# Performance work log

Hardware: AMD Instinct MI355X
Metric: run time of the kernel (lower is better)

## Reference

```python
import jax, jax.numpy as jnp
import numpy as np

B = 4
IN_DIM = 512
HID = 1024
MLP_LAYERS = 2
SEQ = 4096          # output_dim / sequence_length
RH = 64             # ripl_hidden_dim
RL = 2              # ripl_num_layers
MULT = 1            # ripl_coordinate_multipler

MID_DIM = 2 * RH * RH + (RH + 1) * RH      # per middle ripple layer param count
OUT_DIM = 2 * RH * 1 + (RH + 1) * 1        # output ripple layer param count
MLP_OUT = RL * MID_DIM + OUT_DIM


def gelu(x):
    return jax.nn.gelu(x, approximate=False)


def layer_norm(x, g, b, eps=1e-5):
    mu = jnp.mean(x, axis=-1, keepdims=True)
    var = jnp.var(x, axis=-1, keepdims=True)
    return (x - mu) * jax.lax.rsqrt(var + eps) * g + b


def batch_ripple(x, w, b):
    # x: (B,S,I), w: (B,O,I,2), b: (B,O,I+1)
    # out[b,s,o] = b[b,o,0] + sum_i b[b,o,i+1] * sin(w[b,o,i,0]*x[b,s,i] + w[b,o,i,1])
    arg = w[:, None, :, :, 0] * x[:, :, None, :] + w[:, None, :, :, 1]  # (B,S,O,I)
    return b[:, None, :, 0] + jnp.sum(jnp.sin(arg) * b[:, None, :, 1:], axis=-1)


def setup_inputs() -> dict:
    key = jax.random.key(0)
    ks = jax.random.split(key, 20)
    s = 0.02
    inp = {
        "x": jax.random.normal(ks[0], (B, IN_DIM), jnp.float32),
        "mlp_w0": jax.random.normal(ks[1], (IN_DIM, HID), jnp.float32) * s,
        "mlp_b0": jnp.zeros((HID,), jnp.float32),
        "mlp_w1": jax.random.normal(ks[2], (HID, HID), jnp.float32) * s,
        "mlp_b1": jnp.zeros((HID,), jnp.float32),
        "ln_g1": jnp.ones((HID,), jnp.float32),
        "ln_b1": jnp.zeros((HID,), jnp.float32),
        "mlp_w2": jax.random.normal(ks[3], (HID, HID), jnp.float32) * s,
        "mlp_b2": jnp.zeros((HID,), jnp.float32),
        "ln_g2": jnp.ones((HID,), jnp.float32),
        "ln_b2": jnp.zeros((HID,), jnp.float32),
        "mlp_w3": jax.random.normal(ks[4], (HID, MLP_OUT), jnp.float32) * s,
        "mlp_b3": jnp.zeros((MLP_OUT,), jnp.float32),
        "lc_w": jax.random.normal(ks[5], (1, RH), jnp.float32) * 0.1,
        "lc_b": jax.random.normal(ks[6], (RH,), jnp.float32) * 0.1,
        "byp_w": jax.random.normal(ks[7], (1, 1, 2), jnp.float32),
        "byp_b": jax.random.normal(ks[8], (1, 2), jnp.float32),
    }
    return inp


def reference(x, mlp_w0, mlp_b0, mlp_w1, mlp_b1, ln_g1, ln_b1,
              mlp_w2, mlp_b2, ln_g2, ln_b2, mlp_w3, mlp_b3,
              lc_w, lc_b, byp_w, byp_b):
    # hypernetwork MLP: Linear+GELU, [Linear+LN+GELU]*2, Linear
    h = gelu(x @ mlp_w0 + mlp_b0)
    h = gelu(layer_norm(h @ mlp_w1 + mlp_b1, ln_g1, ln_b1))
    h = gelu(layer_norm(h @ mlp_w2 + mlp_b2, ln_g2, ln_b2))
    mlp_out = h @ mlp_w3 + mlp_b3                      # (B, MLP_OUT)

    # split into RL middle ripple layers then the output layer
    middles = [mlp_out[:, i * MID_DIM:(i + 1) * MID_DIM] for i in range(RL)]
    out_w = mlp_out[:, RL * MID_DIM:RL * MID_DIM + OUT_DIM]

    # line coordinates -> fc layer
    lc = (jnp.arange(SEQ, dtype=jnp.float32) * MULT)[None, :, None]  # (1,S,1)
    lc = jnp.broadcast_to(lc, (x.shape[0], SEQ, 1))
    lc_x = lc @ lc_w + lc_b                                          # (B,S,RH)
    lc_bypass = lc_x

    for mw in middles:
        w = mw[:, :2 * RH * RH].reshape(-1, RH, RH, 2)
        b = mw[:, 2 * RH * RH:].reshape(-1, RH, RH + 1)
        lc_x = gelu(batch_ripple(lc_x, w, b))

    wo = out_w[:, :2 * RH].reshape(-1, 1, RH, 2)
    bo = out_w[:, 2 * RH:].reshape(-1, 1, RH + 1)
    lc_x = batch_ripple(lc_x, wo, bo)                                # (B,S,1)

    # learned RippleLinear(1,1) bypass, broadcast over features then reduced
    byp = byp_b[0, 0] + jnp.sum(
        jnp.sin(byp_w[0, 0, 0] * lc_bypass + byp_w[0, 0, 1]) * byp_b[0, 1],
        axis=-1, keepdims=True)
    lc_x = lc_x + byp
    return jnp.transpose(lc_x, (0, 2, 1))                            # (B,1,S)
```

## Files before the change

kernel.cpp:

```cpp
#include <hip/hip_runtime.h>
#include <hip/hip_bf16.h>
#include <math.h>

#define B_      4
#define IN_DIM  512
#define HID     1024
#define SEQ     4096
#define RH      64
#define RL      2
#define MID_DIM 12352
#define OUT_DIM 193
#define MLP_OUT 24897
#define INV2PI  0.15915494309189535f

#define MLPT_STRIDE 25088

#define OFF_P0    0
#define OFF_P1    32768
#define OFF_H1    98304
#define OFF_P2    102400
#define OFF_H2    167936
#define OFF_P3    172032
#define OFF_MLPT  968736

__device__ __forceinline__ float gelu_exact(float v) {
    return 0.5f * v * (1.0f + erff(v * 0.70710678118654752f));
}

__device__ __forceinline__ float hw_sin_rev(float r) {
    r = r - __builtin_rintf(r);
    return __builtin_amdgcn_sinf(r);
}

__global__ void k_gemm0(const float* __restrict__ x, const float* __restrict__ w0,
                        float* __restrict__ p0) {
    const int cch = blockIdx.x;
    const int kc  = blockIdx.y;
    const int tid = threadIdx.x;
    __shared__ float xs[256];
    {
        const int b = tid >> 6, k = tid & 63;
        xs[tid] = x[b * IN_DIM + kc * 64 + k];
    }
    __syncthreads();
    const int b = tid >> 6, cl = tid & 63;
    const int c = cch * 64 + cl;
    const float* wp = w0 + (size_t)(kc * 64) * HID + c;
    const float* xp = xs + b * 64;
    float acc = 0.f;
    #pragma unroll 8
    for (int k = 0; k < 64; ++k)
        acc = fmaf(xp[k], wp[(size_t)k * HID], acc);
    p0[(kc * 4 + b) * HID + c] = acc;
}

__global__ void k_gemm1(const float* __restrict__ p0, const float* __restrict__ b0,
                        const float* __restrict__ w1, float* __restrict__ p1) {
    const int cch = blockIdx.x;
    const int kc  = blockIdx.y;
    const int tid = threadIdx.x;
    __shared__ float hs[256];
    {
        const int b = tid >> 6, k = tid & 63;
        const int kg = kc * 64 + k;
        float v = b0[kg];
        #pragma unroll
        for (int j = 0; j < 8; ++j) v += p0[(j * 4 + b) * HID + kg];
        hs[tid] = gelu_exact(v);
    }
    __syncthreads();
    const int b = tid >> 6, cl = tid & 63;
    const int c = cch * 64 + cl;
    const float* wp = w1 + (size_t)(kc * 64) * HID + c;
    const float* hp = hs + b * 64;
    float acc = 0.f;
    #pragma unroll 8
    for (int k = 0; k < 64; ++k)
        acc = fmaf(hp[k], wp[(size_t)k * HID], acc);
    p1[(kc * 4 + b) * HID + c] = acc;
}

__global__ void k_gemm2(const float* __restrict__ h, const float* __restrict__ w,
                        float* __restrict__ pout) {
    const int cch = blockIdx.x;
    const int kc  = blockIdx.y;
    const int tid = threadIdx.x;
    __shared__ float hs[256];
    {
        const int b = tid >> 6, k = tid & 63;
        hs[tid] = h[b * HID + kc * 64 + k];
    }
    __syncthreads();
    const int b = tid >> 6, cl = tid & 63;
    const int c = cch * 64 + cl;
    const float* wp = w + (size_t)(kc * 64) * HID + c;
    const float* hp = hs + b * 64;
    float acc = 0.f;
    #pragma unroll 8
    for (int k = 0; k < 64; ++k)
        acc = fmaf(hp[k], wp[(size_t)k * HID], acc);
    pout[(kc * 4 + b) * HID + c] = acc;
}

__global__ void k_lng(const float* __restrict__ part, const float* __restrict__ bias,
                      const float* __restrict__ g, const float* __restrict__ bl,
                      float* __restrict__ h) {
    const int b = blockIdx.x, tid = threadIdx.x;
    float v = bias[tid];
    #pragma unroll
    for (int j = 0; j < 16; ++j) v += part[(j * 4 + b) * HID + tid];
    float s1 = v, s2 = v * v;
    #pragma unroll
    for (int m = 1; m < 64; m <<= 1) {
        s1 += __shfl_xor(s1, m, 64);
        s2 += __shfl_xor(s2, m, 64);
    }
    __shared__ float r1[16], r2[16], s_mu, s_rs;
    const int lane = tid & 63, wid = tid >> 6;
    if (lane == 0) { r1[wid] = s1; r2[wid] = s2; }
    __syncthreads();
    if (tid == 0) {
        float a = 0.f, c = 0.f;
        #pragma unroll
        for (int j = 0; j < 16; ++j) { a += r1[j]; c += r2[j]; }
        const float mu = a * (1.0f / HID);
        s_mu = mu;
        s_rs = rsqrtf(c * (1.0f / HID) - mu * mu + 1e-5f);
    }
    __syncthreads();
    h[b * HID + tid] = gelu_exact((v - s_mu) * s_rs * g[tid] + bl[tid]);
}

__global__ void k_gemm3(const float* __restrict__ h2, const float* __restrict__ w3,
                        float* __restrict__ p3) {
    const int cch = blockIdx.x;
    const int kc  = blockIdx.y;
    const int tid = threadIdx.x;
    __shared__ float hs[512];
    for (int e = tid; e < 512; e += 256) {
        const int b = e >> 7, k = e & 127;
        hs[e] = h2[b * HID + kc * 128 + k];
    }
    __syncthreads();
    const int c = cch * 256 + tid;
    if (c >= MLP_OUT) return;
    const float* wp = w3 + (size_t)(kc * 128) * MLP_OUT + c;
    float a0 = 0.f, a1 = 0.f, a2 = 0.f, a3 = 0.f;
    #pragma unroll 16
    for (int k = 0; k < 128; ++k) {
        const float w = wp[(size_t)k * MLP_OUT];
        a0 = fmaf(hs[k],       w, a0);
        a1 = fmaf(hs[128 + k], w, a1);
        a2 = fmaf(hs[256 + k], w, a2);
        a3 = fmaf(hs[384 + k], w, a3);
    }
    p3[(size_t)(kc * 4 + 0) * MLP_OUT + c] = a0;
    p3[(size_t)(kc * 4 + 1) * MLP_OUT + c] = a1;
    p3[(size_t)(kc * 4 + 2) * MLP_OUT + c] = a2;
    p3[(size_t)(kc * 4 + 3) * MLP_OUT + c] = a3;
}

__global__ void k_comb3T(const float* __restrict__ p3, const float* __restrict__ b3,
                         float* __restrict__ mlpT) {
    const int d = blockIdx.x * 256 + threadIdx.x;
    const int b = blockIdx.y;
    int src = -1;
    float scale = 1.f;
    if (d < 24832) {
        const int l = d / 12416, r = d % 12416;
        const int base = l * MID_DIM;
        if (r < 8192) {
            const int half = r >> 12;
            const int rr = r & 4095;
            const int i = rr >> 6, o = rr & 63;
            src = base + o * 128 + i * 2 + half;
            scale = INV2PI;
        } else if (r < 12288) {
            const int rr = r - 8192;
            const int i = rr >> 6, o = rr & 63;
            src = base + 8192 + o * 65 + 1 + i;
        } else if (r < 12352) {
            const int o = r - 12288;
            src = base + 8192 + o * 65;
        }
    } else {
        const int rr = d - 24832;
        const int base = RL * MID_DIM;
        if (rr < 64)        { src = base + rr * 2;            scale = INV2PI; }
        else if (rr < 128)  { src = base + (rr - 64) * 2 + 1; scale = INV2PI; }
        else if (rr < 192)  { src = base + 128 + 1 + (rr - 128); }
        else if (rr == 192) { src = base + 128; }
    }
    float v = 0.f;
    if (src >= 0) {
        v = b3[src];
        #pragma unroll
        for (int j = 0; j < 8; ++j) v += p3[(size_t)(j * 4 + b) * MLP_OUT + src];
        v *= scale;
    }
    mlpT[(size_t)b * MLPT_STRIDE + d] = v;
}

__global__ void __launch_bounds__(256, 2) k_ripple(
        const float* __restrict__ mlpT, const float* __restrict__ lcw,
        const float* __restrict__ lcb, const float* __restrict__ bypw,
        const float* __restrict__ bypb, float* __restrict__ out) {
    const int tid = threadIdx.x;
    const int b = blockIdx.y;
    const int t0 = blockIdx.x * 32;
    const int lane = tid & 63, wid = tid >> 6, tb = wid * 8;

    __shared__ __align__(16) float s_w[12416];
    __shared__ __align__(16) float s_x[64 * 36];
    __shared__ __align__(16) float s_wo[256];
    __shared__ float s_red[32];

    const float* mb = mlpT + (size_t)b * MLPT_STRIDE;

    {
        const float4* src = reinterpret_cast<const float4*>(mb);
        float4* dst = reinterpret_cast<float4*>(s_w);
        for (int e = tid; e < 3104; e += 256) dst[e] = src[e];
        if (tid < 64) {
            reinterpret_cast<float4*>(s_wo)[tid] =
                reinterpret_cast<const float4*>(mb + 24832)[tid];
        }
    }
    const float lw = lcw[lane], lb = lcb[lane];
    for (int e = tid; e < 2048; e += 256) {
        const int i = e >> 5, tt = e & 31;
        s_x[i * 36 + tt] = fmaf((float)(t0 + tt), lcw[i], lcb[i]);
    }
    __syncthreads();

    float acc[8];
    for (int layer = 0; layer < 2; ++layer) {
        const float bc = s_w[12288 + lane];
        #pragma unroll
        for (int j = 0; j < 8; ++j) acc[j] = bc;
        for (int i = 0; i < 64; ++i) {
            const float ws = s_w[i * 64 + lane];
            const float wo = s_w[4096 + i * 64 + lane];
            const float bs = s_w[8192 + i * 64 + lane];
            const float4 xa = *reinterpret_cast<const float4*>(&s_x[i * 36 + tb]);
            const float4 xb = *reinterpret_cast<const float4*>(&s_x[i * 36 + tb + 4]);
            const float xv[8] = {xa.x, xa.y, xa.z, xa.w, xb.x, xb.y, xb.z, xb.w};
            #pragma unroll
            for (int j = 0; j < 8; ++j) {
                const float r = fmaf(ws, xv[j], wo);
                acc[j] = fmaf(hw_sin_rev(r), bs, acc[j]);
            }
        }
        __syncthreads();
        if (layer == 0) {
            #pragma unroll
            for (int j = 0; j < 8; ++j)
                s_x[lane * 36 + tb + j] = gelu_exact(acc[j]);
            const float4* src = reinterpret_cast<const float4*>(mb + 12416);
            float4* dst = reinterpret_cast<float4*>(s_w);
            for (int e = tid; e < 3104; e += 256) dst[e] = src[e];
            __syncthreads();
        }
    }

    {
        const float wsO = s_wo[lane], woO = s_wo[64 + lane], bsO = s_wo[128 + lane];
        const float bcO = s_wo[192];
        const float bw0 = bypw[0] * INV2PI, bw1 = bypw[1] * INV2PI;
        const float bb0 = bypb[0], bb1 = bypb[1];
        #pragma unroll
        for (int j = 0; j < 8; ++j) {
            const int t = t0 + tb + j;
            const float v = gelu_exact(acc[j]);
            float s = hw_sin_rev(fmaf(wsO, v, woO)) * bsO;
            const float xb = fmaf((float)t, lw, lb);
            s = fmaf(hw_sin_rev(fmaf(bw0, xb, bw1)), bb1, s);
            #pragma unroll
            for (int m = 1; m < 64; m <<= 1) s += __shfl_xor(s, m, 64);
            if (lane == 0) s_red[tb + j] = s + bcO + bb0;
        }
    }
    __syncthreads();
    if (tid < 32) out[(size_t)b * SEQ + t0 + tid] = s_red[tid];
}

extern "C" void kernel_launch(void* const* d_in, const int* in_sizes, int n_in,
                              void* d_out, int out_size, void* d_ws, size_t ws_size,
                              hipStream_t stream) {
    const float* x     = (const float*)d_in[0];
    const float* w0    = (const float*)d_in[1];
    const float* b0    = (const float*)d_in[2];
    const float* w1    = (const float*)d_in[3];
    const float* b1    = (const float*)d_in[4];
    const float* g1    = (const float*)d_in[5];
    const float* bln1  = (const float*)d_in[6];
    const float* w2    = (const float*)d_in[7];
    const float* b2    = (const float*)d_in[8];
    const float* g2    = (const float*)d_in[9];
    const float* bln2  = (const float*)d_in[10];
    const float* w3    = (const float*)d_in[11];
    const float* b3    = (const float*)d_in[12];
    const float* lcw   = (const float*)d_in[13];
    const float* lcb   = (const float*)d_in[14];
    const float* bypw  = (const float*)d_in[15];
    const float* bypb  = (const float*)d_in[16];
    float* out = (float*)d_out;
    float* ws  = (float*)d_ws;

    float* p0   = ws + OFF_P0;
    float* p1   = ws + OFF_P1;
    float* h1   = ws + OFF_H1;
    float* p2   = ws + OFF_P2;
    float* h2   = ws + OFF_H2;
    float* p3   = ws + OFF_P3;
    float* mlpT = ws + OFF_MLPT;

    k_gemm0 <<<dim3(16, 8),  256, 0, stream>>>(x,  w0, p0);
    k_gemm1 <<<dim3(16, 16), 256, 0, stream>>>(p0, b0, w1, p1);
    k_lng   <<<B_, 1024,     0, stream>>>(p1, b1, g1, bln1, h1);
    k_gemm2 <<<dim3(16, 16), 256, 0, stream>>>(h1, w2, p2);
    k_lng   <<<B_, 1024,     0, stream>>>(p2, b2, g2, bln2, h2);
    k_gemm3 <<<dim3(98, 8),  256, 0, stream>>>(h2, w3, p3);
    k_comb3T<<<dim3(98, B_), 256, 0, stream>>>(p3, b3, mlpT);
    k_ripple<<<dim3(SEQ / 32, B_), 256, 0, stream>>>(mlpT, lcw, lcb, bypw, bypb, out);
}
```

Measured before the change: 262.5 us.

## Fuse MLP and ripple stages into one cooperative persistent kernel with grid syncs

Replaces the eight separate launches with one cooperative kernel of 512 blocks that runs each stage in turn, separated by grid.sync(). Gemm3 is restructured so each block covers all of K for 64 columns, reducing partials in shared memory and writing the transposed, pre-scaled ripple parameters directly, which removes the separate combine kernel and the p3 round trip. The goal is to cut launch overhead and inter-kernel gaps. In exchange there are several grid-wide barriers, and occupancy is limited by about 60KB of shared memory per block. If the cooperative launch fails, it falls back to the multi-kernel path.

```diff
diff --git a/kernel.cpp b/kernel.cpp
--- a/kernel.cpp
+++ b/kernel.cpp
@@ -1,6 +1,8 @@
 #include <hip/hip_runtime.h>
-#include <hip/hip_bf16.h>
+#include <hip/hip_cooperative_groups.h>
 #include <math.h>
+
+namespace cg = cooperative_groups;
 
 #define B_      4
 #define IN_DIM  512
@@ -12,7 +14,6 @@
 #define OUT_DIM 193
 #define MLP_OUT 24897
 #define INV2PI  0.15915494309189535f
-
 #define MLPT_STRIDE 25088
 
 #define OFF_P0    0
@@ -20,8 +21,8 @@
 #define OFF_H1    98304
 #define OFF_P2    102400
 #define OFF_H2    167936
-#define OFF_P3    172032
-#define OFF_MLPT  968736
+#define OFF_MLPT  172032
+#define OFF_P3F   272384
 
 __device__ __forceinline__ float gelu_exact(float v) {
     return 0.5f * v * (1.0f + erff(v * 0.70710678118654752f));
@@ -32,16 +33,271 @@
     return __builtin_amdgcn_sinf(r);
 }
 
+__device__ __forceinline__ void lng_phase(const float* __restrict__ part,
+                                          const float* __restrict__ bias,
+                                          const float* __restrict__ g,
+                                          const float* __restrict__ bl,
+                                          float* __restrict__ h,
+                                          int b, int tid, float* smem) {
+    float v[4];
+    float s1 = 0.f, s2 = 0.f;
+    #pragma unroll
+    for (int q = 0; q < 4; ++q) {
+        const int col = q * 256 + tid;
+        float t = bias[col];
+        #pragma unroll
+        for (int j = 0; j < 16; ++j) t += part[(j * 4 + b) * HID + col];
+        v[q] = t; s1 += t; s2 += t * t;
+    }
+    #pragma unroll
+    for (int m = 1; m < 64; m <<= 1) {
+        s1 += __shfl_xor(s1, m, 64);
+        s2 += __shfl_xor(s2, m, 64);
+    }
+    const int lane = tid & 63, wid = tid >> 6;
+    if (lane == 0) { smem[wid] = s1; smem[4 + wid] = s2; }
+    __syncthreads();
+    if (tid == 0) {
+        float a = 0.f, c = 0.f;
+        #pragma unroll
+        for (int j = 0; j < 4; ++j) { a += smem[j]; c += smem[4 + j]; }
+        const float mu = a * (1.0f / HID);
+        smem[8] = mu;
+        smem[9] = rsqrtf(c * (1.0f / HID) - mu * mu + 1e-5f);
+    }
+    __syncthreads();
+    const float mu = smem[8], rs = smem[9];
+    #pragma unroll
+    for (int q = 0; q < 4; ++q) {
+        const int col = q * 256 + tid;
+        h[b * HID + col] = gelu_exact((v[q] - mu) * rs * g[col] + bl[col]);
+    }
+}
+
+__global__ void __launch_bounds__(256, 2) k_fused(
+        const float* __restrict__ x,   const float* __restrict__ w0,
+        const float* __restrict__ b0,  const float* __restrict__ w1,
+        const float* __restrict__ b1,  const float* __restrict__ g1,
+        const float* __restrict__ bl1, const float* __restrict__ w2,
+        const float* __restrict__ b2,  const float* __restrict__ g2,
+        const float* __restrict__ bl2, const float* __restrict__ w3,
+        const float* __restrict__ b3,  const float* __restrict__ lcw,
+        const float* __restrict__ lcb, const float* __restrict__ bypw,
+        const float* __restrict__ bypb, float* __restrict__ out,
+        float* __restrict__ ws) {
+    cg::grid_group grid = cg::this_grid();
+    const int bid = blockIdx.x;
+    const int tid = threadIdx.x;
+    __shared__ __align__(16) float smem[15008];
+
+    float* p0   = ws + OFF_P0;
+    float* p1   = ws + OFF_P1;
+    float* h1   = ws + OFF_H1;
+    float* p2   = ws + OFF_P2;
+    float* h2   = ws + OFF_H2;
+    float* mlpT = ws + OFF_MLPT;
+
+    if (bid < 128) {
+        const int kc = bid >> 4, cch = bid & 15;
+        float* xs = smem;
+        { const int b = tid >> 6, k = tid & 63; xs[tid] = x[b * IN_DIM + kc * 64 + k]; }
+        __syncthreads();
+        const int b = tid >> 6, cl = tid & 63;
+        const int c = cch * 64 + cl;
+        const float* wp = w0 + (size_t)(kc * 64) * HID + c;
+        const float* xp = xs + b * 64;
+        float acc = 0.f;
+        #pragma unroll 8
+        for (int k = 0; k < 64; ++k) acc = fmaf(xp[k], wp[(size_t)k * HID], acc);
+        p0[(kc * 4 + b) * HID + c] = acc;
+    }
+    grid.sync();
+
+    if (bid < 256) {
+        const int kc = bid >> 4, cch = bid & 15;
+        float* hs = smem;
+        {
+            const int b = tid >> 6, k = tid & 63;
+            const int kg = kc * 64 + k;
+            float v = b0[kg];
+            #pragma unroll
+            for (int j = 0; j < 8; ++j) v += p0[(j * 4 + b) * HID + kg];
+            hs[tid] = gelu_exact(v);
+        }
+        __syncthreads();
+        const int b = tid >> 6, cl = tid & 63;
+        const int c = cch * 64 + cl;
+        const float* wp = w1 + (size_t)(kc * 64) * HID + c;
+        const float* hp = hs + b * 64;
+        float acc = 0.f;
+        #pragma unroll 8
+        for (int k = 0; k < 64; ++k) acc = fmaf(hp[k], wp[(size_t)k * HID], acc);
+        p1[(kc * 4 + b) * HID + c] = acc;
+    }
+    grid.sync();
+
+    if (bid < 4) lng_phase(p1, b1, g1, bl1, h1, bid, tid, smem);
+    grid.sync();
+
+    if (bid < 256) {
+        const int kc = bid >> 4, cch = bid & 15;
+        float* hs = smem;
+        {
+            const int b = tid >> 6, k = tid & 63;
+            hs[tid] = h1[b * HID + kc * 64 + k];
+        }
+        __syncthreads();
+        const int b = tid >> 6, cl = tid & 63;
+        const int c = cch * 64 + cl;
+        const float* wp = w2 + (size_t)(kc * 64) * HID + c;
+        const float* hp = hs + b * 64;
+        float acc = 0.f;
+        #pragma unroll 8
+        for (int k = 0; k < 64; ++k) acc = fmaf(hp[k], wp[(size_t)k * HID], acc);
+        p2[(kc * 4 + b) * HID + c] = acc;
+    }
+    grid.sync();
+
+    if (bid < 4) lng_phase(p2, b2, g2, bl2, h2, bid, tid, smem);
+    grid.sync();
+
+    if (bid < 390) {
+        float* sh  = smem;
+        float* red = smem + 4096;
+        for (int e = tid; e < 4096; e += 256) sh[e] = h2[e];
+        __syncthreads();
+        const int cl = tid & 63, kg = tid >> 6;
+        const int c = bid * 64 + cl;
+        float a0 = 0.f, a1 = 0.f, a2 = 0.f, a3 = 0.f;
+        if (c < MLP_OUT) {
+            const float* wp = w3 + (size_t)(kg * 256) * MLP_OUT + c;
+            const float* h0 = sh + kg * 256;
+            #pragma unroll 16
+            for (int k = 0; k < 256; ++k) {
+                const float w = wp[(size_t)k * MLP_OUT];
+                a0 = fmaf(h0[k],        w, a0);
+                a1 = fmaf(h0[1024 + k], w, a1);
+                a2 = fmaf(h0[2048 + k], w, a2);
+                a3 = fmaf(h0[3072 + k], w, a3);
+            }
+        }
+        red[(kg * 4 + 0) * 64 + cl] = a0;
+        red[(kg * 4 + 1) * 64 + cl] = a1;
+        red[(kg * 4 + 2) * 64 + cl] = a2;
+        red[(kg * 4 + 3) * 64 + cl] = a3;
+        __syncthreads();
+        if (c < MLP_OUT) {
+            float v = b3[c];
+            #pragma unroll
+            for (int j = 0; j < 4; ++j) v += red[(j * 4 + kg) * 64 + cl];
+            int d; float scale = 1.f;
+            if (c < RL * MID_DIM) {
+                const int l = c / MID_DIM, r = c % MID_DIM;
+                if (r < 8192) {
+                    const int o = r >> 7, rem = r & 127;
+                    d = l * 12416 + (rem & 1) * 4096 + (rem >> 1) * 64 + o;
+                    scale = INV2PI;
+                } else {
+                    const int u = r - 8192;
+                    const int o = u / 65, idx = u % 65;
+                    d = l * 12416 + (idx == 0 ? 12288 + o : 8192 + (idx - 1) * 64 + o);
+                }
+            } else {
+                const int u = c - RL * MID_DIM;
+                if (u < 128)      { d = 24832 + (u & 1) * 64 + (u >> 1); scale = INV2PI; }
+                else if (u == 128){ d = 24832 + 192; }
+                else              { d = 24832 + 128 + (u - 129); }
+            }
+            mlpT[(size_t)kg * MLPT_STRIDE + d] = v * scale;
+        }
+    }
+    grid.sync();
+
+    {
+        const int b  = bid & 3;
+        const int t0 = (bid >> 2) * 32;
+        const int lane = tid & 63, wid = tid >> 6, tb = wid * 8;
+
+        float* s_w   = smem;
+        float* s_x   = smem + 12416;
+        float* s_wo  = smem + 14720;
+        float* s_red = smem + 14976;
+
+        const float* mb = mlpT + (size_t)b * MLPT_STRIDE;
+
+        {
+            const float4* src = reinterpret_cast<const float4*>(mb);
+            float4* dst = reinterpret_cast<float4*>(s_w);
+            for (int e = tid; e < 3104; e += 256) dst[e] = src[e];
+            if (tid < 64) {
+                reinterpret_cast<float4*>(s_wo)[tid] =
+                    reinterpret_cast<const float4*>(mb + 24832)[tid];
+            }
+        }
+        const float lw = lcw[lane], lb = lcb[lane];
+        for (int e = tid; e < 2048; e += 256) {
+            const int i = e >> 5, tt = e & 31;
+            s_x[i * 36 + tt] = fmaf((float)(t0 + tt), lcw[i], lcb[i]);
+        }
+        __syncthreads();
+
+        float acc[8];
+        for (int layer = 0; layer < 2; ++layer) {
+            const float bc = s_w[12288 + lane];
+            #pragma unroll
+            for (int j = 0; j < 8; ++j) acc[j] = bc;
+            for (int i = 0; i < 64; ++i) {
+                const float ws_ = s_w[i * 64 + lane];
+                const float wo_ = s_w[4096 + i * 64 + lane];
+                const float bs_ = s_w[8192 + i * 64 + lane];
+                const float4 xa = *reinterpret_cast<const float4*>(&s_x[i * 36 + tb]);
+                const float4 xb = *reinterpret_cast<const float4*>(&s_x[i * 36 + tb + 4]);
+                const float xv[8] = {xa.x, xa.y, xa.z, xa.w, xb.x, xb.y, xb.z, xb.w};
+                #pragma unroll
+                for (int j = 0; j < 8; ++j) {
+                    const float r = fmaf(ws_, xv[j], wo_);
+                    acc[j] = fmaf(hw_sin_rev(r), bs_, acc[j]);
+                }
+            }
+            __syncthreads();
+            if (layer == 0) {
+                #pragma unroll
+                for (int j = 0; j < 8; ++j)
+                    s_x[lane * 36 + tb + j] = gelu_exact(acc[j]);
+                const float4* src = reinterpret_cast<const float4*>(mb + 12416);
+                float4* dst = reinterpret_cast<float4*>(s_w);
+                for (int e = tid; e < 3104; e += 256) dst[e] = src[e];
+                __syncthreads();
+            }
+        }
+
+        {
+            const float wsO = s_wo[lane], woO = s_wo[64 + lane], bsO = s_wo[128 + lane];
+            const float bcO = s_wo[192];
+            const float bw0 = bypw[0] * INV2PI, bw1 = bypw[1] * INV2PI;
+            const float bb0 = bypb[0], bb1 = bypb[1];
+            #pragma unroll
+            for (int j = 0; j < 8; ++j) {
+                const int t = t0 + tb + j;
+                const float v = gelu_exact(acc[j]);
+                float s = hw_sin_rev(fmaf(wsO, v, woO)) * bsO;
+                const float xbv = fmaf((float)t, lw, lb);
+                s = fmaf(hw_sin_rev(fmaf(bw0, xbv, bw1)), bb1, s);
+                #pragma unroll
+                for (int m = 1; m < 64; m <<= 1) s += __shfl_xor(s, m, 64);
+                if (lane == 0) s_red[tb + j] = s + bcO + bb0;
+            }
+        }
+        __syncthreads();
+        if (tid < 32) out[(size_t)b * SEQ + t0 + tid] = s_red[tid];
+    }
+}
+
 __global__ void k_gemm0(const float* __restrict__ x, const float* __restrict__ w0,
                         float* __restrict__ p0) {
-    const int cch = blockIdx.x;
-    const int kc  = blockIdx.y;
-    const int tid = threadIdx.x;
+    const int cch = blockIdx.x, kc = blockIdx.y, tid = threadIdx.x;
     __shared__ float xs[256];
-    {
-        const int b = tid >> 6, k = tid & 63;
-        xs[tid] = x[b * IN_DIM + kc * 64 + k];
-    }
+    { const int b = tid >> 6, k = tid & 63; xs[tid] = x[b * IN_DIM + kc * 64 + k]; }
     __syncthreads();
     const int b = tid >> 6, cl = tid & 63;
     const int c = cch * 64 + cl;
@@ -49,16 +305,13 @@
     const float* xp = xs + b * 64;
     float acc = 0.f;
     #pragma unroll 8
-    for (int k = 0; k < 64; ++k)
-        acc = fmaf(xp[k], wp[(size_t)k * HID], acc);
+    for (int k = 0; k < 64; ++k) acc = fmaf(xp[k], wp[(size_t)k * HID], acc);
     p0[(kc * 4 + b) * HID + c] = acc;
 }
 
 __global__ void k_gemm1(const float* __restrict__ p0, const float* __restrict__ b0,
                         const float* __restrict__ w1, float* __restrict__ p1) {
-    const int cch = blockIdx.x;
-    const int kc  = blockIdx.y;
-    const int tid = threadIdx.x;
+    const int cch = blockIdx.x, kc = blockIdx.y, tid = threadIdx.x;
     __shared__ float hs[256];
     {
         const int b = tid >> 6, k = tid & 63;
@@ -75,21 +328,15 @@
     const float* hp = hs + b * 64;
     float acc = 0.f;
     #pragma unroll 8
-    for (int k = 0; k < 64; ++k)
-        acc = fmaf(hp[k], wp[(size_t)k * HID], acc);
+    for (int k = 0; k < 64; ++k) acc = fmaf(hp[k], wp[(size_t)k * HID], acc);
     p1[(kc * 4 + b) * HID + c] = acc;
 }
 
 __global__ void k_gemm2(const float* __restrict__ h, const float* __restrict__ w,
                         float* __restrict__ pout) {
-    const int cch = blockIdx.x;
-    const int kc  = blockIdx.y;
-    const int tid = threadIdx.x;
+    const int cch = blockIdx.x, kc = blockIdx.y, tid = threadIdx.x;
     __shared__ float hs[256];
-    {
-        const int b = tid >> 6, k = tid & 63;
-        hs[tid] = h[b * HID + kc * 64 + k];
-    }
+    { const int b = tid >> 6, k = tid & 63; hs[tid] = h[b * HID + kc * 64 + k]; }
     __syncthreads();
     const int b = tid >> 6, cl = tid & 63;
     const int c = cch * 64 + cl;
@@ -97,8 +344,7 @@
     const float* hp = hs + b * 64;
     float acc = 0.f;
     #pragma unroll 8
-    for (int k = 0; k < 64; ++k)
-        acc = fmaf(hp[k], wp[(size_t)k * HID], acc);
+    for (int k = 0; k < 64; ++k) acc = fmaf(hp[k], wp[(size_t)k * HID], acc);
     pout[(kc * 4 + b) * HID + c] = acc;
 }
 
@@ -133,9 +379,7 @@
 
 __global__ void k_gemm3(const float* __restrict__ h2, const float* __restrict__ w3,
                         float* __restrict__ p3) {
-    const int cch = blockIdx.x;
-    const int kc  = blockIdx.y;
-    const int tid = threadIdx.x;
+    const int cch = blockIdx.x, kc = blockIdx.y, tid = threadIdx.x;
     __shared__ float hs[512];
     for (int e = tid; e < 512; e += 256) {
         const int b = e >> 7, k = e & 127;
@@ -239,16 +483,16 @@
         #pragma unroll
         for (int j = 0; j < 8; ++j) acc[j] = bc;
         for (int i = 0; i < 64; ++i) {
-            const float ws = s_w[i * 64 + lane];
-            const float wo = s_w[4096 + i * 64 + lane];
-            const float bs = s_w[8192 + i * 64 + lane];
+            const float ws_ = s_w[i * 64 + lane];
+            const float wo_ = s_w[4096 + i * 64 + lane];
+            const float bs_ = s_w[8192 + i * 64 + lane];
             const float4 xa = *reinterpret_cast<const float4*>(&s_x[i * 36 + tb]);
             const float4 xb = *reinterpret_cast<const float4*>(&s_x[i * 36 + tb + 4]);
             const float xv[8] = {xa.x, xa.y, xa.z, xa.w, xb.x, xb.y, xb.z, xb.w};
             #pragma unroll
             for (int j = 0; j < 8; ++j) {
-                const float r = fmaf(ws, xv[j], wo);
-                acc[j] = fmaf(hw_sin_rev(r), bs, acc[j]);
+                const float r = fmaf(ws_, xv[j], wo_);
+                acc[j] = fmaf(hw_sin_rev(r), bs_, acc[j]);
             }
         }
         __syncthreads();
@@ -273,8 +517,8 @@
             const int t = t0 + tb + j;
             const float v = gelu_exact(acc[j]);
             float s = hw_sin_rev(fmaf(wsO, v, woO)) * bsO;
-            const float xb = fmaf((float)t, lw, lb);
-            s = fmaf(hw_sin_rev(fmaf(bw0, xb, bw1)), bb1, s);
+            const float xbv = fmaf((float)t, lw, lb);
+            s = fmaf(hw_sin_rev(fmaf(bw0, xbv, bw1)), bb1, s);
             #pragma unroll
             for (int m = 1; m < 64; m <<= 1) s += __shfl_xor(s, m, 64);
             if (lane == 0) s_red[tb + j] = s + bcO + bb0;
@@ -307,20 +551,30 @@
     float* out = (float*)d_out;
     float* ws  = (float*)d_ws;
 
-    float* p0   = ws + OFF_P0;
-    float* p1   = ws + OFF_P1;
-    float* h1   = ws + OFF_H1;
-    float* p2   = ws + OFF_P2;
-    float* h2   = ws + OFF_H2;
-    float* p3   = ws + OFF_P3;
-    float* mlpT = ws + OFF_MLPT;
-
-    k_gemm0 <<<dim3(16, 8),  256, 0, stream>>>(x,  w0, p0);
-    k_gemm1 <<<dim3(16, 16), 256, 0, stream>>>(p0, b0, w1, p1);
-    k_lng   <<<B_, 1024,     0, stream>>>(p1, b1, g1, bln1, h1);
-    k_gemm2 <<<dim3(16, 16), 256, 0, stream>>>(h1, w2, p2);
-    k_lng   <<<B_, 1024,     0, stream>>>(p2, b2, g2, bln2, h2);
-    k_gemm3 <<<dim3(98, 8),  256, 0, stream>>>(h2, w3, p3);
-    k_comb3T<<<dim3(98, B_), 256, 0, stream>>>(p3, b3, mlpT);
-    k_ripple<<<dim3(SEQ / 32, B_), 256, 0, stream>>>(mlpT, lcw, lcb, bypw, bypb, out);
-}
+    void* args[] = {
+        (void*)&x, (void*)&w0, (void*)&b0, (void*)&w1, (void*)&b1,
+        (void*)&g1, (void*)&bln1, (void*)&w2, (void*)&b2, (void*)&g2,
+        (void*)&bln2, (void*)&w3, (void*)&b3, (void*)&lcw, (void*)&lcb,
+        (void*)&bypw, (void*)&bypb, (void*)&out, (void*)&ws
+    };
+    hipError_t err = hipLaunchCooperativeKernel((const void*)k_fused,
+                                                dim3(512), dim3(256),
+                                                args, 0, stream);
+    if (err != hipSuccess) {
+        float* p0   = ws + OFF_P0;
+        float* p1   = ws + OFF_P1;
+        float* h1   = ws + OFF_H1;
+        float* p2   = ws + OFF_P2;
+        float* h2   = ws + OFF_H2;
+        float* mlpT = ws + OFF_MLPT;
+        float* p3   = ws + OFF_P3F;
+        k_gemm0 <<<dim3(16, 8),  256, 0, stream>>>(x,  w0, p0);
+        k_gemm1 <<<dim3(16, 16), 256, 0, stream>>>(p0, b0, w1, p1);
+        k_lng   <<<B_, 1024,     0, stream>>>(p1, b1, g1, bln1, h1);
+        k_gemm2 <<<dim3(16, 16), 256, 0, stream>>>(h1, w2, p2);
+        k_lng   <<<B_, 1024,     0, stream>>>(p2, b2, g2, bln2, h2);
+        k_gemm3 <<<dim3(98, 8),  256, 0, stream>>>(h2, w3, p3);
+        k_comb3T<<<dim3(98, B_), 256, 0, stream>>>(p3, b3, mlpT);
+        k_ripple<<<dim3(SEQ / 32, B_), 256, 0, stream>>>(mlpT, lcw, lcb, bypw, bypb, out);
+    }
+}
```

After: 576.9 us. 120% more time.

## Fuse MLP stages into three kernels with redundant layernorm and in-block K reduction

Applied to the files above, without the earlier changes.

Collapses the eight-kernel MLP pipeline into three kernels plus the ripple kernel. gemm0 is fused into gemm1 by having each block recompute its own 64-wide slice of the first hidden layer. Each layernorm is recomputed per block, inside the following GEMM or the final projection. The final projection reduces its K split in shared memory and writes the transposed, scaled ripple parameters directly. This removes launch overhead and the partial-sum round trips through global memory, at the cost of redundant work: gemm0 is recomputed 16 times and each layernorm reduction is repeated in every block.

```diff
diff --git a/kernel.cpp b/kernel.cpp
--- a/kernel.cpp
+++ b/kernel.cpp
@@ -1,5 +1,4 @@
 #include <hip/hip_runtime.h>
-#include <hip/hip_bf16.h>
 #include <math.h>
 
 #define B_      4
@@ -12,16 +11,11 @@
 #define OUT_DIM 193
 #define MLP_OUT 24897
 #define INV2PI  0.15915494309189535f
-
 #define MLPT_STRIDE 25088
 
-#define OFF_P0    0
-#define OFF_P1    32768
-#define OFF_H1    98304
-#define OFF_P2    102400
-#define OFF_H2    167936
-#define OFF_P3    172032
-#define OFF_MLPT  968736
+#define OFF_P1    0
+#define OFF_P2    65536
+#define OFF_MLPT  131072
 
 __device__ __forceinline__ float gelu_exact(float v) {
     return 0.5f * v * (1.0f + erff(v * 0.70710678118654752f));
@@ -32,173 +26,169 @@
     return __builtin_amdgcn_sinf(r);
 }
 
-__global__ void k_gemm0(const float* __restrict__ x, const float* __restrict__ w0,
-                        float* __restrict__ p0) {
-    const int cch = blockIdx.x;
-    const int kc  = blockIdx.y;
-    const int tid = threadIdx.x;
-    __shared__ float xs[256];
-    {
-        const int b = tid >> 6, k = tid & 63;
-        xs[tid] = x[b * IN_DIM + kc * 64 + k];
-    }
-    __syncthreads();
-    const int b = tid >> 6, cl = tid & 63;
-    const int c = cch * 64 + cl;
-    const float* wp = w0 + (size_t)(kc * 64) * HID + c;
-    const float* xp = xs + b * 64;
-    float acc = 0.f;
-    #pragma unroll 8
-    for (int k = 0; k < 64; ++k)
-        acc = fmaf(xp[k], wp[(size_t)k * HID], acc);
-    p0[(kc * 4 + b) * HID + c] = acc;
-}
-
-__global__ void k_gemm1(const float* __restrict__ p0, const float* __restrict__ b0,
-                        const float* __restrict__ w1, float* __restrict__ p1) {
-    const int cch = blockIdx.x;
-    const int kc  = blockIdx.y;
-    const int tid = threadIdx.x;
-    __shared__ float hs[256];
-    {
-        const int b = tid >> 6, k = tid & 63;
-        const int kg = kc * 64 + k;
-        float v = b0[kg];
-        #pragma unroll
-        for (int j = 0; j < 8; ++j) v += p0[(j * 4 + b) * HID + kg];
-        hs[tid] = gelu_exact(v);
-    }
-    __syncthreads();
-    const int b = tid >> 6, cl = tid & 63;
-    const int c = cch * 64 + cl;
-    const float* wp = w1 + (size_t)(kc * 64) * HID + c;
-    const float* hp = hs + b * 64;
-    float acc = 0.f;
-    #pragma unroll 8
-    for (int k = 0; k < 64; ++k)
-        acc = fmaf(hp[k], wp[(size_t)k * HID], acc);
-    p1[(kc * 4 + b) * HID + c] = acc;
-}
-
-__global__ void k_gemm2(const float* __restrict__ h, const float* __restrict__ w,
-                        float* __restrict__ pout) {
-    const int cch = blockIdx.x;
-    const int kc  = blockIdx.y;
-    const int tid = threadIdx.x;
-    __shared__ float hs[256];
-    {
-        const int b = tid >> 6, k = tid & 63;
-        hs[tid] = h[b * HID + kc * 64 + k];
-    }
-    __syncthreads();
-    const int b = tid >> 6, cl = tid & 63;
-    const int c = cch * 64 + cl;
-    const float* wp = w + (size_t)(kc * 64) * HID + c;
-    const float* hp = hs + b * 64;
-    float acc = 0.f;
-    #pragma unroll 8
-    for (int k = 0; k < 64; ++k)
-        acc = fmaf(hp[k], wp[(size_t)k * HID], acc);
-    pout[(kc * 4 + b) * HID + c] = acc;
-}
-
-__global__ void k_lng(const float* __restrict__ part, const float* __restrict__ bias,
-                      const float* __restrict__ g, const float* __restrict__ bl,
-                      float* __restrict__ h) {
-    const int b = blockIdx.x, tid = threadIdx.x;
-    float v = bias[tid];
+__global__ void __launch_bounds__(256) k_A(
+        const float* __restrict__ x,  const float* __restrict__ w0,
+        const float* __restrict__ b0, const float* __restrict__ w1,
+        float* __restrict__ p1) {
+    const int cch = blockIdx.x, kc = blockIdx.y, tid = threadIdx.x;
+    __shared__ __align__(16) float xs[B_ * IN_DIM];
+    __shared__ float h0s[256];
+
+    for (int e = tid; e < B_ * IN_DIM; e += 256) xs[e] = x[e];
+    __syncthreads();
+
+    {
+        const int b = tid >> 6, kgl = tid & 63;
+        const int kg = kc * 64 + kgl;
+        const float* xp = xs + b * IN_DIM;
+        const float* wp = w0 + kg;
+        float acc = 0.f;
+        #pragma unroll 8
+        for (int k = 0; k < IN_DIM; ++k)
+            acc = fmaf(xp[k], wp[(size_t)k * HID], acc);
+        h0s[tid] = gelu_exact(acc + b0[kg]);
+    }
+    __syncthreads();
+
+    {
+        const int b = tid >> 6, cl = tid & 63;
+        const int c = cch * 64 + cl;
+        const float* wp = w1 + (size_t)(kc * 64) * HID + c;
+        const float* hp = h0s + b * 64;
+        float acc = 0.f;
+        #pragma unroll 8
+        for (int k = 0; k < 64; ++k)
+            acc = fmaf(hp[k], wp[(size_t)k * HID], acc);
+        p1[(kc * 4 + b) * HID + c] = acc;
+    }
+}
+
+__global__ void __launch_bounds__(256) k_B(
+        const float* __restrict__ p1, const float* __restrict__ b1,
+        const float* __restrict__ g1, const float* __restrict__ bl1,
+        const float* __restrict__ w2, float* __restrict__ p2) {
+    const int cch = blockIdx.x, kc = blockIdx.y, tid = threadIdx.x;
+    __shared__ float h1s[256];
+    const int b = tid >> 6, lane = tid & 63;
+
+    float s1 = 0.f, s2 = 0.f;
     #pragma unroll
-    for (int j = 0; j < 16; ++j) v += part[(j * 4 + b) * HID + tid];
-    float s1 = v, s2 = v * v;
+    for (int q = 0; q < 16; ++q) {
+        const int c = q * 64 + lane;
+        float v = b1[c];
+        #pragma unroll
+        for (int j = 0; j < 16; ++j) v += p1[(j * 4 + b) * HID + c];
+        s1 += v; s2 += v * v;
+    }
     #pragma unroll
     for (int m = 1; m < 64; m <<= 1) {
         s1 += __shfl_xor(s1, m, 64);
         s2 += __shfl_xor(s2, m, 64);
     }
-    __shared__ float r1[16], r2[16], s_mu, s_rs;
-    const int lane = tid & 63, wid = tid >> 6;
-    if (lane == 0) { r1[wid] = s1; r2[wid] = s2; }
-    __syncthreads();
-    if (tid == 0) {
-        float a = 0.f, c = 0.f;
-        #pragma unroll
-        for (int j = 0; j < 16; ++j) { a += r1[j]; c += r2[j]; }
-        const float mu = a * (1.0f / HID);
-        s_mu = mu;
-        s_rs = rsqrtf(c * (1.0f / HID) - mu * mu + 1e-5f);
-    }
-    __syncthreads();
-    h[b * HID + tid] = gelu_exact((v - s_mu) * s_rs * g[tid] + bl[tid]);
-}
-
-__global__ void k_gemm3(const float* __restrict__ h2, const float* __restrict__ w3,
-                        float* __restrict__ p3) {
-    const int cch = blockIdx.x;
-    const int kc  = blockIdx.y;
-    const int tid = threadIdx.x;
-    __shared__ float hs[512];
-    for (int e = tid; e < 512; e += 256) {
-        const int b = e >> 7, k = e & 127;
-        hs[e] = h2[b * HID + kc * 128 + k];
-    }
-    __syncthreads();
-    const int c = cch * 256 + tid;
-    if (c >= MLP_OUT) return;
-    const float* wp = w3 + (size_t)(kc * 128) * MLP_OUT + c;
+    const float mu = s1 * (1.0f / HID);
+    const float rs = rsqrtf(s2 * (1.0f / HID) - mu * mu + 1e-5f);
+
+    {
+        const int k = kc * 64 + lane;
+        float v = b1[k];
+        #pragma unroll
+        for (int j = 0; j < 16; ++j) v += p1[(j * 4 + b) * HID + k];
+        h1s[tid] = gelu_exact((v - mu) * rs * g1[k] + bl1[k]);
+    }
+    __syncthreads();
+
+    {
+        const int c = cch * 64 + lane;
+        const float* wp = w2 + (size_t)(kc * 64) * HID + c;
+        const float* hp = h1s + b * 64;
+        float acc = 0.f;
+        #pragma unroll 8
+        for (int k = 0; k < 64; ++k)
+            acc = fmaf(hp[k], wp[(size_t)k * HID], acc);
+        p2[(kc * 4 + b) * HID + c] = acc;
+    }
+}
+
+__global__ void __launch_bounds__(256) k_C(
+        const float* __restrict__ p2, const float* __restrict__ b2,
+        const float* __restrict__ g2, const float* __restrict__ bl2,
+        const float* __restrict__ w3, const float* __restrict__ b3,
+        float* __restrict__ mlpT) {
+    const int bid = blockIdx.x, tid = threadIdx.x;
+    __shared__ __align__(16) float h2s[B_ * HID];
+    __shared__ float red[1024];
+
+    {
+        const int b = tid >> 6, lane = tid & 63;
+        float s1 = 0.f, s2 = 0.f;
+        float vv[16];
+        #pragma unroll
+        for (int q = 0; q < 16; ++q) {
+            const int c = q * 64 + lane;
+            float v = b2[c];
+            #pragma unroll
+            for (int j = 0; j < 16; ++j) v += p2[(j * 4 + b) * HID + c];
+            vv[q] = v; s1 += v; s2 += v * v;
+        }
+        #pragma unroll
+        for (int m = 1; m < 64; m <<= 1) {
+            s1 += __shfl_xor(s1, m, 64);
+            s2 += __shfl_xor(s2, m, 64);
+        }
+        const float mu = s1 * (1.0f / HID);
+        const float rs = rsqrtf(s2 * (1.0f / HID) - mu * mu + 1e-5f);
+        #pragma unroll
+        for (int q = 0; q < 16; ++q) {
+            const int c = q * 64 + lane;
+            h2s[b * HID + c] = gelu_exact((vv[q] - mu) * rs * g2[c] + bl2[c]);
+        }
+    }
+    __syncthreads();
+
+    const int cl = tid & 63, kg = tid >> 6;
+    const int c = bid * 64 + cl;
     float a0 = 0.f, a1 = 0.f, a2 = 0.f, a3 = 0.f;
-    #pragma unroll 16
-    for (int k = 0; k < 128; ++k) {
-        const float w = wp[(size_t)k * MLP_OUT];
-        a0 = fmaf(hs[k],       w, a0);
-        a1 = fmaf(hs[128 + k], w, a1);
-        a2 = fmaf(hs[256 + k], w, a2);
-        a3 = fmaf(hs[384 + k], w, a3);
-    }
-    p3[(size_t)(kc * 4 + 0) * MLP_OUT + c] = a0;
-    p3[(size_t)(kc * 4 + 1) * MLP_OUT + c] = a1;
-    p3[(size_t)(kc * 4 + 2) * MLP_OUT + c] = a2;
-    p3[(size_t)(kc * 4 + 3) * MLP_OUT + c] = a3;
-}
-
-__global__ void k_comb3T(const float* __restrict__ p3, const float* __restrict__ b3,
-                         float* __restrict__ mlpT) {
-    const int d = blockIdx.x * 256 + threadIdx.x;
-    const int b = blockIdx.y;
-    int src = -1;
-    float scale = 1.f;
-    if (d < 24832) {
-        const int l = d / 12416, r = d % 12416;
-        const int base = l * MID_DIM;
-        if (r < 8192) {
-            const int half = r >> 12;
-            const int rr = r & 4095;
-            const int i = rr >> 6, o = rr & 63;
-            src = base + o * 128 + i * 2 + half;
-            scale = INV2PI;
-        } else if (r < 12288) {
-            const int rr = r - 8192;
-            const int i = rr >> 6, o = rr & 63;
-            src = base + 8192 + o * 65 + 1 + i;
-        } else if (r < 12352) {
-            const int o = r - 12288;
-            src = base + 8192 + o * 65;
-        }
-    } else {
-        const int rr = d - 24832;
-        const int base = RL * MID_DIM;
-        if (rr < 64)        { src = base + rr * 2;            scale = INV2PI; }
-        else if (rr < 128)  { src = base + (rr - 64) * 2 + 1; scale = INV2PI; }
-        else if (rr < 192)  { src = base + 128 + 1 + (rr - 128); }
-        else if (rr == 192) { src = base + 128; }
-    }
-    float v = 0.f;
-    if (src >= 0) {
-        v = b3[src];
-        #pragma unroll
-        for (int j = 0; j < 8; ++j) v += p3[(size_t)(j * 4 + b) * MLP_OUT + src];
-        v *= scale;
-    }
-    mlpT[(size_t)b * MLPT_STRIDE + d] = v;
+    if (c < MLP_OUT) {
+        const float* wp = w3 + (size_t)(kg * 256) * MLP_OUT + c;
+        const float* h0 = h2s + kg * 256;
+        #pragma unroll 16
+        for (int k = 0; k < 256; ++k) {
+            const float w = wp[(size_t)k * MLP_OUT];
+            a0 = fmaf(h0[k],        w, a0);
+            a1 = fmaf(h0[1024 + k], w, a1);
+            a2 = fmaf(h0[2048 + k], w, a2);
+            a3 = fmaf(h0[3072 + k], w, a3);
+        }
+    }
+    red[(kg * 4 + 0) * 64 + cl] = a0;
+    red[(kg * 4 + 1) * 64 + cl] = a1;
+    red[(kg * 4 + 2) * 64 + cl] = a2;
+    red[(kg * 4 + 3) * 64 + cl] = a3;
+    __syncthreads();
+    if (c < MLP_OUT) {
+        float v = b3[c];
+        #pragma unroll
+        for (int j = 0; j < 4; ++j) v += red[(j * 4 + kg) * 64 + cl];
+        int d; float scale = 1.f;
+        if (c < RL * MID_DIM) {
+            const int l = c / MID_DIM, r = c % MID_DIM;
+            if (r < 8192) {
+                const int o = r >> 7, rem = r & 127;
+                d = l * 12416 + (rem & 1) * 4096 + (rem >> 1) * 64 + o;
+                scale = INV2PI;
+            } else {
+                const int u = r - 8192;
+                const int o = u / 65, idx = u % 65;
+                d = l * 12416 + (idx == 0 ? 12288 + o : 8192 + (idx - 1) * 64 + o);
+            }
+        } else {
+            const int u = c - RL * MID_DIM;
+            if (u < 128)      { d = 24832 + (u & 1) * 64 + (u >> 1); scale = INV2PI; }
+            else if (u == 128){ d = 24832 + 192; }
+            else              { d = 24832 + 128 + (u - 129); }
+        }
+        mlpT[(size_t)kg * MLPT_STRIDE + d] = v * scale;
+    }
 }
 
 __global__ void __launch_bounds__(256, 2) k_ripple(
@@ -239,16 +229,16 @@
         #pragma unroll
         for (int j = 0; j < 8; ++j) acc[j] = bc;
         for (int i = 0; i < 64; ++i) {
-            const float ws = s_w[i * 64 + lane];
-            const float wo = s_w[4096 + i * 64 + lane];
-            const float bs = s_w[8192 + i * 64 + lane];
+            const float ws_ = s_w[i * 64 + lane];
+            const float wo_ = s_w[4096 + i * 64 + lane];
+            const float bs_ = s_w[8192 + i * 64 + lane];
             const float4 xa = *reinterpret_cast<const float4*>(&s_x[i * 36 + tb]);
             const float4 xb = *reinterpret_cast<const float4*>(&s_x[i * 36 + tb + 4]);
             const float xv[8] = {xa.x, xa.y, xa.z, xa.w, xb.x, xb.y, xb.z, xb.w};
             #pragma unroll
             for (int j = 0; j < 8; ++j) {
-                const float r = fmaf(ws, xv[j], wo);
-                acc[j] = fmaf(hw_sin_rev(r), bs, acc[j]);
+                const float r = fmaf(ws_, xv[j], wo_);
+                acc[j] = fmaf(hw_sin_rev(r), bs_, acc[j]);
             }
         }
         __syncthreads();
@@ -273,8 +263,8 @@
             const int t = t0 + tb + j;
             const float v = gelu_exact(acc[j]);
             float s = hw_sin_rev(fmaf(wsO, v, woO)) * bsO;
-            const float xb = fmaf((float)t, lw, lb);
-            s = fmaf(hw_sin_rev(fmaf(bw0, xb, bw1)), bb1, s);
+            const float xbv = fmaf((float)t, lw, lb);
+            s = fmaf(hw_sin_rev(fmaf(bw0, xbv, bw1)), bb1, s);
             #pragma unroll
             for (int m = 1; m < 64; m <<= 1) s += __shfl_xor(s, m, 64);
             if (lane == 0) s_red[tb + j] = s + bcO + bb0;
@@ -307,20 +297,12 @@
     float* out = (float*)d_out;
     float* ws  = (float*)d_ws;
 
-    float* p0   = ws + OFF_P0;
     float* p1   = ws + OFF_P1;
-    float* h1   = ws + OFF_H1;
     float* p2   = ws + OFF_P2;
-    float* h2   = ws + OFF_H2;
-    float* p3   = ws + OFF_P3;
     float* mlpT = ws + OFF_MLPT;
 
-    k_gemm0 <<<dim3(16, 8),  256, 0, stream>>>(x,  w0, p0);
-    k_gemm1 <<<dim3(16, 16), 256, 0, stream>>>(p0, b0, w1, p1);
-    k_lng   <<<B_, 1024,     0, stream>>>(p1, b1, g1, bln1, h1);
-    k_gemm2 <<<dim3(16, 16), 256, 0, stream>>>(h1, w2, p2);
-    k_lng   <<<B_, 1024,     0, stream>>>(p2, b2, g2, bln2, h2);
-    k_gemm3 <<<dim3(98, 8),  256, 0, stream>>>(h2, w3, p3);
-    k_comb3T<<<dim3(98, B_), 256, 0, stream>>>(p3, b3, mlpT);
-    k_ripple<<<dim3(SEQ / 32, B_), 256, 0, stream>>>(mlpT, lcw, lcb, bypw, bypb, out);
-}
+    k_A     <<<dim3(16, 16),      256, 0, stream>>>(x, w0, b0, w1, p1);
+    k_B     <<<dim3(16, 16),      256, 0, stream>>>(p1, b1, g1, bln1, w2, p2);
+    k_C     <<<dim3(390),         256, 0, stream>>>(p2, b2, g2, bln2, w3, b3, mlpT);
+    k_ripple<<<dim3(SEQ / 32, B_),256, 0, stream>>>(mlpT, lcw, lcb, bypw, bypb, out);
+}
```

Result: slower. 342.5 us (+30.5%).
